# Kernel tuning notes

Hardware: AMD Instinct MI355X
Metric: run time of the kernel (lower is better)

Reference implementation:

```python
import jax, jax.numpy as jnp
import numpy as np

N_KNN = 16
BN_EPS = 1e-5


def conv1d(x, w, b):
    # x: (B,Cin,N), w: (Cout,Cin) -> (B,Cout,N)
    return jnp.einsum('oc,bcn->bon', w, x) + b[None, :, None]


def conv2d(x, w, b):
    # x: (B,Cin,N,K), w: (Cout,Cin) -> (B,Cout,N,K)
    return jnp.einsum('oc,bcnk->bonk', w, x) + b[None, :, None, None]


def bn2d(x, gamma, beta):
    # training-mode BatchNorm2d over (B,N,K) per channel
    mu = x.mean(axis=(0, 2, 3), keepdims=True)
    var = x.var(axis=(0, 2, 3), keepdims=True)
    return (x - mu) * jax.lax.rsqrt(var + BN_EPS) * gamma[None, :, None, None] + beta[None, :, None, None]


def knn_idx(pos, k):
    # pos: (B,3,N) -> (B,N,K) indices of k nearest neighbors (include_self=True)
    p = jnp.transpose(pos, (0, 2, 1))  # (B,N,3)
    sq = jnp.sum(p * p, axis=-1)  # (B,N)
    d = sq[:, :, None] + sq[:, None, :] - 2.0 * jnp.einsum('bnd,bmd->bnm', p, p)
    _, idx = jax.lax.top_k(-d, k)
    return idx


def group(feat, idx):
    # feat: (B,C,N), idx: (B,N,K) -> (B,C,N,K)
    return jnp.take_along_axis(feat[:, :, :, None], idx[:, None, :, :], axis=2)


def mlp_res(x, w1, b1, w2, b2, wsc, bsc):
    shortcut = conv1d(x, wsc, bsc)
    return conv1d(jax.nn.relu(conv1d(x, w1, b1)), w2, b2) + shortcut


def setup_inputs() -> dict:
    key0 = jax.random.key(0)
    ks = jax.random.split(key0, 16)
    B, N, C, D, PH = 2, 2048, 128, 256, 64
    AH = D * 4
    f = lambda i, shape: jax.random.normal(ks[i], shape, jnp.float32) * 0.02
    return dict(
        pos=jax.random.normal(ks[0], (B, 3, N), jnp.float32),
        key=jax.random.normal(ks[1], (B, C, N), jnp.float32),
        query=jax.random.normal(ks[2], (B, C, N), jnp.float32),
        mlp_w1=f(3, (C, 2 * C)), mlp_b1=jnp.zeros(C),
        mlp_w2=f(4, (C, C)), mlp_b2=jnp.zeros(C),
        mlp_wsc=f(5, (C, 2 * C)), mlp_bsc=jnp.zeros(C),
        wk=f(6, (D, C)), bk=jnp.zeros(D),
        wq=f(7, (D, C)), bq=jnp.zeros(D),
        wv=f(8, (D, C)), bv=jnp.zeros(D),
        pos_w1=f(9, (PH, 3)), pos_b1=jnp.zeros(PH),
        pos_g=jnp.ones(PH), pos_beta=jnp.zeros(PH),
        pos_w2=f(10, (D, PH)), pos_b2=jnp.zeros(D),
        attn_w1=f(11, (AH, D)), attn_b1=jnp.zeros(AH),
        attn_g=jnp.ones(AH), attn_beta=jnp.zeros(AH),
        attn_w2=f(12, (D, AH)), attn_b2=jnp.zeros(D),
        end_w=f(13, (C, D)), end_b=jnp.zeros(C),
    )


def reference(pos, key, query,
              mlp_w1, mlp_b1, mlp_w2, mlp_b2, mlp_wsc, mlp_bsc,
              wk, bk, wq, bq, wv, bv,
              pos_w1, pos_b1, pos_g, pos_beta, pos_w2, pos_b2,
              attn_w1, attn_b1, attn_g, attn_beta, attn_w2, attn_b2,
              end_w, end_b):
    # value = MLP_Res(cat(key, query))
    value = mlp_res(jnp.concatenate([key, query], axis=1),
                    mlp_w1, mlp_b1, mlp_w2, mlp_b2, mlp_wsc, mlp_bsc)
    identity = value
    k = conv1d(key, wk, bk)      # (B,D,N)
    q = conv1d(query, wq, bq)    # (B,D,N)
    v = conv1d(value, wv, bv)    # (B,D,N)

    idx = knn_idx(pos, N_KNN)    # (B,N,K)
    key_g = group(k, idx)        # (B,D,N,K)
    qk_rel = q[:, :, :, None] - key_g
    pos_rel = pos[:, :, :, None] - group(pos, idx)  # (B,3,N,K)

    # pos_mlp: conv2d -> BN -> ReLU -> conv2d
    h = jax.nn.relu(bn2d(conv2d(pos_rel, pos_w1, pos_b1), pos_g, pos_beta))
    pos_emb = conv2d(h, pos_w2, pos_b2)  # (B,D,N,K)

    # attn_mlp: conv2d -> BN -> ReLU -> conv2d, softmax over neighbor axis
    a = jax.nn.relu(bn2d(conv2d(qk_rel + pos_emb, attn_w1, attn_b1), attn_g, attn_beta))
    attn = jax.nn.softmax(conv2d(a, attn_w2, attn_b2), axis=-1)  # (B,D,N,K)

    val = v[:, :, :, None] + pos_emb
    agg = jnp.sum(attn * val, axis=-1)  # (B,D,N)
    y = conv1d(agg, end_w, end_b)
    return y + identity
```

## Files before the change

kernel.cpp:

```cpp
#include <hip/hip_runtime.h>
#include <hip/hip_bf16.h>
#include <math.h>

#define Bv 2
#define Nv 2048
#define Cv 128
#define Dv 256
#define PHv 64
#define AHv 1024
#define Kv 16
#define NSAMP (Bv*Nv*Kv)

typedef unsigned short ushortt;
typedef unsigned char u8;
typedef __attribute__((ext_vector_type(8))) short bf16x8;
typedef __attribute__((ext_vector_type(4))) float f32x4;

__device__ __forceinline__ float bf2f(ushortt h){
  union { unsigned int u; float f; } v; v.u = ((unsigned int)h) << 16; return v.f;
}
__device__ __forceinline__ ushortt f2bf(float f){
  union { unsigned int u; float f; } v; v.f = f;
  unsigned int r = v.u + 0x7FFFu + ((v.u >> 16) & 1u);
  return (ushortt)(r >> 16);
}
__device__ __forceinline__ u8 f2fp8(float f){
  union { float f; unsigned int u; } v; v.f = f;
  unsigned int s = (v.u >> 24) & 0x80u;
  unsigned int a = v.u & 0x7FFFFFFFu;
  if (a > 0x43E00000u) a = 0x43E00000u;
  unsigned int r = a + 0x7FFFFu + ((a >> 20) & 1u);
  int e = (int)((r >> 23) & 0xFF) - 120;
  unsigned int m = (r >> 20) & 7u;
  if (e <= 0) return (u8)s;
  return (u8)(s | ((unsigned)e << 3) | m);
}

__device__ __forceinline__ void gload16(const void* g, void* l){
  __builtin_amdgcn_global_load_lds(
      (const __attribute__((address_space(1))) unsigned int*)g,
      (__attribute__((address_space(3))) unsigned int*)l, 16, 0, 0);
}

__global__ __launch_bounds__(256) void prep_weights(
    const float* __restrict__ wk, const float* __restrict__ wq,
    const float* __restrict__ wv, const float* __restrict__ endw,
    const float* __restrict__ mw1, const float* __restrict__ mw2,
    const float* __restrict__ mwsc, const float* __restrict__ aw2,
    const float* __restrict__ pw2,
    ushortt* __restrict__ wA16, ushortt* __restrict__ wB16, ushortt* __restrict__ wv16,
    float* __restrict__ endwT, u8* __restrict__ w2f8, ushortt* __restrict__ pw2R)
{
  int tid = blockIdx.x*256 + threadIdx.x;
  int stride = gridDim.x*256;
  for (int i = tid; i < 768*256; i += stride){
    int r = i >> 8, c = i & 255;
    float v;
    if (r < 128) v = mw1[r*256 + c];
    else if (r < 384) v = (c < 128) ? wk[(r-128)*128 + c] : 0.f;
    else if (r < 640) v = (c >= 128) ? wq[(r-384)*128 + (c-128)] : 0.f;
    else v = 0.f;
    wA16[i] = f2bf(v);
  }
  for (int i = tid; i < 128*384; i += stride){
    int r = i / 384, c = i - r*384;
    float v = (c < 128) ? mw2[r*128 + c] : mwsc[r*256 + (c-128)];
    wB16[i] = f2bf(v);
  }
  for (int i = tid; i < 256*128; i += stride) wv16[i] = f2bf(wv[i]);
  for (int i = tid; i < 128*256; i += stride){ int co = i>>8, d = i&255; endwT[d*128+co] = endw[i]; }
  for (int i = tid; i < 256*1024; i += stride) w2f8[i] = f2fp8(aw2[i]*256.f);
  for (int i = tid; i < 256*64; i += stride) pw2R[i] = f2bf(pw2[i]);
}

__global__ __launch_bounds__(256) void xcat_kernel(
    const float* __restrict__ key, const float* __restrict__ query,
    ushortt* __restrict__ hx16)
{
  __shared__ float xs[256*33];
  int t = threadIdx.x;
  int tile = blockIdx.x & 63, b = blockIdx.x >> 6;
  int n0 = tile*32;
  for (int e = t; e < 256*32; e += 256){
    int c = e >> 5, nn = e & 31;
    xs[c*33+nn] = (c < 128) ? key[(size_t)(b*128+c)*Nv + n0+nn]
                            : query[(size_t)(b*128+(c-128))*Nv + n0+nn];
  }
  __syncthreads();
  int nn = t & 31, cg = t >> 5;
  size_t s = (size_t)b*Nv + n0 + nn;
  __align__(16) ushortt tmp[32];
  #pragma unroll
  for (int cc = 0; cc < 32; cc++) tmp[cc] = f2bf(xs[(cg*32+cc)*33 + nn]);
  uint4* dst = (uint4*)&hx16[s*384 + 128 + cg*32];
  #pragma unroll
  for (int q = 0; q < 4; q++) dst[q] = ((uint4*)tmp)[q];
}

__global__ __launch_bounds__(512) void gemmA_kernel(
    ushortt* __restrict__ hx16, const ushortt* __restrict__ wA16,
    const float* __restrict__ mb1, const float* __restrict__ bk, const float* __restrict__ bq,
    float* __restrict__ kT, float* __restrict__ qT)
{
  __shared__ ushortt As[128*64];
  __shared__ ushortt Bs[256*64];
  int t = threadIdx.x;
  int w = t >> 6, l = t & 63;
  int lr = l & 15, g4 = l >> 4;
  int wm = w >> 2, wn = w & 3;
  int s0 = blockIdx.x*128, n0 = blockIdx.y*256;

  f32x4 acc[4][4];
  #pragma unroll
  for (int i=0;i<4;i++) for (int j=0;j<4;j++) acc[i][j] = (f32x4){0.f,0.f,0.f,0.f};

  for (int kt = 0; kt < 4; kt++){
    int k0 = kt*64;
    __syncthreads();
    #pragma unroll
    for (int i = 0; i < 2; i++){
      int c = t + i*512;
      int r = c >> 3, db = (c & 7)*16;
      const ushortt* src = hx16 + (size_t)(s0+r)*384 + 128 + k0 + ((db ^ ((r&7)<<4))>>1);
      gload16(src, As + c*8);
    }
    #pragma unroll
    for (int i = 0; i < 4; i++){
      int c = t + i*512;
      int r = c >> 3, db = (c & 7)*16;
      const ushortt* src = wA16 + (size_t)(n0+r)*256 + k0 + ((db ^ ((r&7)<<4))>>1);
      gload16(src, Bs + c*8);
    }
    __syncthreads();
    #pragma unroll
    for (int kk = 0; kk < 2; kk++){
      int kb = kk*64 + g4*16;
      bf16x8 af[4];
      #pragma unroll
      for (int mi = 0; mi < 4; mi++){
        int row = wm*64 + mi*16 + lr;
        af[mi] = *(const bf16x8*)((const char*)As + row*128 + (kb ^ ((row&7)<<4)));
      }
      #pragma unroll
      for (int ni = 0; ni < 4; ni++){
        int row = wn*64 + ni*16 + lr;
        bf16x8 bfr = *(const bf16x8*)((const char*)Bs + row*128 + (kb ^ ((row&7)<<4)));
        #pragma unroll
        for (int mi = 0; mi < 4; mi++)
          acc[mi][ni] = __builtin_amdgcn_mfma_f32_16x16x32_bf16(af[mi], bfr, acc[mi][ni], 0,0,0);
      }
    }
  }
  #pragma unroll
  for (int ni = 0; ni < 4; ni++){
    int col = n0 + wn*64 + ni*16 + lr;
    if (col < 128){
      float bias = mb1[col];
      #pragma unroll
      for (int mi = 0; mi < 4; mi++){
        int rbase = s0 + wm*64 + mi*16 + g4*4;
        #pragma unroll
        for (int r = 0; r < 4; r++){
          float v = acc[mi][ni][r] + bias;
          v = v > 0.f ? v : 0.f;
          hx16[(size_t)(rbase+r)*384 + col] = f2bf(v);
        }
      }
    } else if (col < 384){
      float bias = bk[col-128];
      #pragma unroll
      for (int mi = 0; mi < 4; mi++){
        int rbase = s0 + wm*64 + mi*16 + g4*4;
        #pragma unroll
        for (int r = 0; r < 4; r++)
          kT[(size_t)(rbase+r)*256 + (col-128)] = acc[mi][ni][r] + bias;
      }
    } else if (col < 640){
      float bias = bq[col-384];
      #pragma unroll
      for (int mi = 0; mi < 4; mi++){
        int rbase = s0 + wm*64 + mi*16 + g4*4;
        #pragma unroll
        for (int r = 0; r < 4; r++)
          qT[(size_t)(rbase+r)*256 + (col-384)] = acc[mi][ni][r] + bias;
      }
    }
  }
}

__global__ __launch_bounds__(512) void gemmB_kernel(
    const ushortt* __restrict__ hx16, const ushortt* __restrict__ wB16,
    const float* __restrict__ mb2, const float* __restrict__ mbsc,
    float* __restrict__ valueT, ushortt* __restrict__ value16)
{
  __shared__ ushortt As[128*64];
  __shared__ ushortt Bs[128*64];
  int t = threadIdx.x;
  int w = t >> 6, l = t & 63;
  int lr = l & 15, g4 = l >> 4;
  int wm = w >> 2, wn = w & 3;
  int s0 = blockIdx.x*128;

  f32x4 acc[4][2];
  #pragma unroll
  for (int i=0;i<4;i++) for (int j=0;j<2;j++) acc[i][j] = (f32x4){0.f,0.f,0.f,0.f};

  for (int kt = 0; kt < 6; kt++){
    int k0 = kt*64;
    __syncthreads();
    #pragma unroll
    for (int i = 0; i < 2; i++){
      int c = t + i*512;
      int r = c >> 3, db = (c & 7)*16;
      const ushortt* src = hx16 + (size_t)(s0+r)*384 + k0 + ((db ^ ((r&7)<<4))>>1);
      gload16(src, As + c*8);
    }
    #pragma unroll
    for (int i = 0; i < 2; i++){
      int c = t + i*512;
      int r = c >> 3, db = (c & 7)*16;
      const ushortt* src = wB16 + (size_t)r*384 + k0 + ((db ^ ((r&7)<<4))>>1);
      gload16(src, Bs + c*8);
    }
    __syncthreads();
    #pragma unroll
    for (int kk = 0; kk < 2; kk++){
      int kb = kk*64 + g4*16;
      bf16x8 af[4];
      #pragma unroll
      for (int mi = 0; mi < 4; mi++){
        int row = wm*64 + mi*16 + lr;
        af[mi] = *(const bf16x8*)((const char*)As + row*128 + (kb ^ ((row&7)<<4)));
      }
      #pragma unroll
      for (int ni = 0; ni < 2; ni++){
        int row = wn*32 + ni*16 + lr;
        bf16x8 bfr = *(const bf16x8*)((const char*)Bs + row*128 + (kb ^ ((row&7)<<4)));
        #pragma unroll
        for (int mi = 0; mi < 4; mi++)
          acc[mi][ni] = __builtin_amdgcn_mfma_f32_16x16x32_bf16(af[mi], bfr, acc[mi][ni], 0,0,0);
      }
    }
  }
  #pragma unroll
  for (int ni = 0; ni < 2; ni++){
    int col = wn*32 + ni*16 + lr;
    float bias = mb2[col] + mbsc[col];
    #pragma unroll
    for (int mi = 0; mi < 4; mi++){
      int rbase = s0 + wm*64 + mi*16 + g4*4;
      #pragma unroll
      for (int r = 0; r < 4; r++){
        float v = acc[mi][ni][r] + bias;
        valueT[(size_t)(rbase+r)*128 + col] = v;
        value16[(size_t)(rbase+r)*128 + col] = f2bf(v);
      }
    }
  }
}

__global__ __launch_bounds__(512) void gemmC_kernel(
    const ushortt* __restrict__ value16, const ushortt* __restrict__ wv16,
    const float* __restrict__ bv, float* __restrict__ vT)
{
  __shared__ ushortt As[128*64];
  __shared__ ushortt Bs[256*64];
  int t = threadIdx.x;
  int w = t >> 6, l = t & 63;
  int lr = l & 15, g4 = l >> 4;
  int wm = w >> 2, wn = w & 3;
  int s0 = blockIdx.x*128;

  f32x4 acc[4][4];
  #pragma unroll
  for (int i=0;i<4;i++) for (int j=0;j<4;j++) acc[i][j] = (f32x4){0.f,0.f,0.f,0.f};

  for (int kt = 0; kt < 2; kt++){
    int k0 = kt*64;
    __syncthreads();
    #pragma unroll
    for (int i = 0; i < 2; i++){
      int c = t + i*512;
      int r = c >> 3, db = (c & 7)*16;
      const ushortt* src = value16 + (size_t)(s0+r)*128 + k0 + ((db ^ ((r&7)<<4))>>1);
      gload16(src, As + c*8);
    }
    #pragma unroll
    for (int i = 0; i < 4; i++){
      int c = t + i*512;
      int r = c >> 3, db = (c & 7)*16;
      const ushortt* src = wv16 + (size_t)r*128 + k0 + ((db ^ ((r&7)<<4))>>1);
      gload16(src, Bs + c*8);
    }
    __syncthreads();
    #pragma unroll
    for (int kk = 0; kk < 2; kk++){
      int kb = kk*64 + g4*16;
      bf16x8 af[4];
      #pragma unroll
      for (int mi = 0; mi < 4; mi++){
        int row = wm*64 + mi*16 + lr;
        af[mi] = *(const bf16x8*)((const char*)As + row*128 + (kb ^ ((row&7)<<4)));
      }
      #pragma unroll
      for (int ni = 0; ni < 4; ni++){
        int row = wn*64 + ni*16 + lr;
        bf16x8 bfr = *(const bf16x8*)((const char*)Bs + row*128 + (kb ^ ((row&7)<<4)));
        #pragma unroll
        for (int mi = 0; mi < 4; mi++)
          acc[mi][ni] = __builtin_amdgcn_mfma_f32_16x16x32_bf16(af[mi], bfr, acc[mi][ni], 0,0,0);
      }
    }
  }
  #pragma unroll
  for (int ni = 0; ni < 4; ni++){
    int col = wn*64 + ni*16 + lr;
    float bias = bv[col];
    #pragma unroll
    for (int mi = 0; mi < 4; mi++){
      int rbase = s0 + wm*64 + mi*16 + g4*4;
      #pragma unroll
      for (int r = 0; r < 4; r++)
        vT[(size_t)(rbase+r)*256 + col] = acc[mi][ni][r] + bias;
    }
  }
}

__global__ __launch_bounds__(256) void knn_kernel(const float* __restrict__ pos, int* __restrict__ idx)
{
  int t = threadIdx.x;
  int w = t >> 6, l = t & 63;
  int p = blockIdx.x*4 + w;
  int i = p & (Nv-1), b = p >> 11;
  const float* px = pos + (size_t)b*3*Nv;
  float pix = px[i], piy = px[Nv+i], piz = px[2*Nv+i];
  float sqi = pix*pix + piy*piy + piz*piz;
  float ds[32];
  #pragma unroll
  for (int jj = 0; jj < 32; jj++){
    int j = jj*64 + l;
    float qx = px[j], qy = px[Nv+j], qz = px[2*Nv+j];
    float sqj = qx*qx + qy*qy + qz*qz;
    float dot = pix*qx + piy*qy + piz*qz;
    ds[jj] = (sqi + sqj) - 2.0f*dot;
  }
  #pragma unroll 1
  for (int it = 0; it < 16; it++){
    float bv = 3.4e38f; int bj = 0x7FFFFFFF;
    #pragma unroll
    for (int jj = 0; jj < 32; jj++){
      int j = jj*64 + l;
      bool c = ds[jj] < bv;
      bv = c ? ds[jj] : bv;
      bj = c ? j : bj;
    }
    #pragma unroll
    for (int off = 32; off; off >>= 1){
      float ov = __shfl_xor(bv, off);
      int oj = __shfl_xor(bj, off);
      if (ov < bv || (ov == bv && oj < bj)){ bv = ov; bj = oj; }
    }
    if (l == 0) idx[(size_t)p*16 + it] = bj;
    #pragma unroll
    for (int jj = 0; jj < 32; jj++){
      if (jj*64 + l == bj) ds[jj] = 3.4e38f;
    }
  }
}

__global__ __launch_bounds__(256) void bn1_stats(const float* __restrict__ pos,
    const int* __restrict__ idx, float* __restrict__ rstat)
{
  int tid = blockIdx.x*256 + threadIdx.x;
  int stride = gridDim.x*256;
  float s[9] = {0,0,0,0,0,0,0,0,0};
  for (int e = tid; e < NSAMP; e += stride){
    int b = e >> 15;
    int rem = e & 32767;
    int n = rem >> 4, k = rem & 15;
    int j = idx[(size_t)(b*Nv+n)*16 + k];
    const float* px = pos + (size_t)b*3*Nv;
    float rx = px[n]-px[j], ry = px[Nv+n]-px[Nv+j], rz = px[2*Nv+n]-px[2*Nv+j];
    s[0]+=rx; s[1]+=ry; s[2]+=rz;
    s[3]+=rx*rx; s[4]+=rx*ry; s[5]+=rx*rz; s[6]+=ry*ry; s[7]+=ry*rz; s[8]+=rz*rz;
  }
  for (int off=32; off; off>>=1)
    for (int q=0;q<9;q++) s[q] += __shfl_xor(s[q], off);
  if ((threadIdx.x & 63) == 0)
    for (int q=0;q<9;q++) atomicAdd(&rstat[q], s[q]);
}

__global__ void bn1_final(const float* __restrict__ rstat,
    const float* __restrict__ pw1,
    const float* __restrict__ pg, const float* __restrict__ pbeta,
    float* __restrict__ w1eff, float* __restrict__ b1eff)
{
  int c = threadIdx.x;
  float inv = 1.0f/(float)NSAMP;
  float mux = rstat[0]*inv, muy = rstat[1]*inv, muz = rstat[2]*inv;
  float xx = rstat[3]*inv, xy = rstat[4]*inv, xz = rstat[5]*inv;
  float yy = rstat[6]*inv, yz = rstat[7]*inv, zz = rstat[8]*inv;
  float w0 = pw1[c*3], w1 = pw1[c*3+1], w2 = pw1[c*3+2];
  float dot = w0*mux + w1*muy + w2*muz;
  float quad = w0*w0*xx + w1*w1*yy + w2*w2*zz + 2.f*(w0*w1*xy + w0*w2*xz + w1*w2*yz);
  float var = quad - dot*dot;
  float s = pg[c] * rsqrtf(var + 1e-5f);
  w1eff[c*3]   = w0*s;
  w1eff[c*3+1] = w1*s;
  w1eff[c*3+2] = w2*s;
  b1eff[c] = pbeta[c] - dot*s;
}

__global__ __launch_bounds__(256) void hpos_kernel(
    const float* __restrict__ pos, const int* __restrict__ idx,
    const float* __restrict__ w1eff, const float* __restrict__ b1eff,
    ushortt* __restrict__ hposR)
{
  int t = threadIdx.x;
  int s = blockIdx.x*32 + (t>>3);
  int c0 = (t&7)*8;
  int ptv = s >> 4;
  int n = ptv & (Nv-1), b = ptv >> 11;
  int j = idx[s];
  const float* px = pos + (size_t)b*3*Nv;
  float rx = px[n]-px[j], ry = px[Nv+n]-px[Nv+j], rz = px[2*Nv+n]-px[2*Nv+j];
  ushortt outv[8];
  #pragma unroll
  for (int e = 0; e < 8; e++){
    int c = c0+e;
    float v = b1eff[c] + w1eff[c*3]*rx + w1eff[c*3+1]*ry + w1eff[c*3+2]*rz;
    outv[e] = f2bf(v > 0.f ? v : 0.f);
  }
  *(uint4*)&hposR[(size_t)s*64 + c0] = *(uint4*)outv;
}

__global__ __launch_bounds__(512) void gemm0_kernel(
    const ushortt* __restrict__ hposR, const ushortt* __restrict__ pw2R,
    const float* __restrict__ pb2, const int* __restrict__ idx,
    const float* __restrict__ qT, const float* __restrict__ kT, const float* __restrict__ vT,
    ushortt* __restrict__ U16, ushortt* __restrict__ val16, float* __restrict__ mu_sum)
{
  __shared__ ushortt As[128*64];
  __shared__ ushortt Bs[256*64];
  __shared__ float mured[8*256];
  int t = threadIdx.x;
  int w = t >> 6, l = t & 63;
  int lr = l & 15, g4 = l >> 4;
  int wm = w >> 2, wn = w & 3;
  int s0 = blockIdx.x*128;

  #pragma unroll
  for (int i = 0; i < 2; i++){
    int c = t + i*512;
    int r = c >> 3, db = (c & 7)*16;
    const ushortt* src = hposR + (size_t)(s0+r)*64 + ((db ^ ((r&7)<<4))>>1);
    gload16(src, As + c*8);
  }
  #pragma unroll
  for (int i = 0; i < 4; i++){
    int c = t + i*512;
    int r = c >> 3, db = (c & 7)*16;
    const ushortt* src = pw2R + (size_t)r*64 + ((db ^ ((r&7)<<4))>>1);
    gload16(src, Bs + c*8);
  }
  __syncthreads();

  f32x4 acc[4][4];
  #pragma unroll
  for (int i=0;i<4;i++) for (int j=0;j<4;j++) acc[i][j] = (f32x4){0.f,0.f,0.f,0.f};
  #pragma unroll
  for (int kk = 0; kk < 2; kk++){
    int kb = kk*64 + g4*16;
    bf16x8 af[4];
    #pragma unroll
    for (int mi = 0; mi < 4; mi++){
      int row = wm*64 + mi*16 + lr;
      af[mi] = *(const bf16x8*)((const char*)As + row*128 + (kb ^ ((row&7)<<4)));
    }
    #pragma unroll
    for (int ni = 0; ni < 4; ni++){
      int row = wn*64 + ni*16 + lr;
      bf16x8 bfr = *(const bf16x8*)((const char*)Bs + row*128 + (kb ^ ((row&7)<<4)));
      #pragma unroll
      for (int mi = 0; mi < 4; mi++)
        acc[mi][ni] = __builtin_amdgcn_mfma_f32_16x16x32_bf16(af[mi], bfr, acc[mi][ni], 0,0,0);
    }
  }

  float musum[4] = {0.f,0.f,0.f,0.f};
  __align__(16) float pb2v[4];
  #pragma unroll
  for (int ni = 0; ni < 4; ni++) pb2v[ni] = pb2[wn*64 + ni*16 + lr];
  #pragma unroll
  for (int mi = 0; mi < 4; mi++){
    #pragma unroll
    for (int r4 = 0; r4 < 4; r4++){
      int s = s0 + wm*64 + mi*16 + g4*4 + r4;
      int ptv = s >> 4;
      int b = s >> 15;
      int j = idx[s];
      const float* krow = kT + (size_t)(b*Nv + j)*256;
      const float* qrow = qT + (size_t)ptv*256;
      const float* vrow = vT + (size_t)ptv*256;
      #pragma unroll
      for (int ni = 0; ni < 4; ni++){
        int d = wn*64 + ni*16 + lr;
        float pe = acc[mi][ni][r4] + pb2v[ni];
        float u = qrow[d] - krow[d] + pe;
        U16[(size_t)s*256 + d] = f2bf(u);
        val16[(size_t)s*256 + d] = f2bf(vrow[d] + pe);
        musum[ni] += u;
      }
    }
  }
  #pragma unroll
  for (int ni = 0; ni < 4; ni++)
    mured[(wm*4+g4)*256 + wn*64 + ni*16 + lr] = musum[ni];
  __syncthreads();
  if (t < 256){
    float ssum = 0.f;
    #pragma unroll
    for (int q = 0; q < 8; q++) ssum += mured[q*256 + t];
    atomicAdd(&mu_sum[t], ssum);
  }
}

__global__ __launch_bounds__(512) void mm_kernel(const ushortt* __restrict__ U16,
                                                 ushortt* __restrict__ Mpart)
{
  __shared__ ushortt Ut[256*64];
  int t = threadIdx.x;
  int w = t >> 6, l = t & 63;
  int lr = l & 15, g4 = l >> 4;
  int wm = w >> 2, wn = w & 3;
  int c_my = ((w & 3)*64 + l);
  int sg = w >> 2;
  int blk = blockIdx.x;
  int sstart = blk*256;

  f32x4 acc[8][4];
  #pragma unroll
  for (int i=0;i<8;i++) for (int j=0;j<4;j++) acc[i][j] = (f32x4){0.f,0.f,0.f,0.f};

  for (int st = 0; st < 4; st++){
    int sb = sstart + st*64;
    __syncthreads();
    #pragma unroll
    for (int g = 0; g < 4; g++){
      int s8 = sg*32 + g*8;
      ushortt vals[8];
      #pragma unroll
      for (int e = 0; e < 8; e++)
        vals[e] = U16[(size_t)(sb + s8 + e)*256 + c_my];
      unsigned int p0 = (unsigned int)vals[0] | ((unsigned int)vals[1] << 16);
      unsigned int p1 = (unsigned int)vals[2] | ((unsigned int)vals[3] << 16);
      unsigned int p2 = (unsigned int)vals[4] | ((unsigned int)vals[5] << 16);
      unsigned int p3 = (unsigned int)vals[6] | ((unsigned int)vals[7] << 16);
      uint4 pk = make_uint4(p0,p1,p2,p3);
      *(uint4*)((char*)Ut + c_my*128 + ((s8*2) ^ ((c_my&7)<<4))) = pk;
    }
    __syncthreads();
    #pragma unroll
    for (int kk = 0; kk < 2; kk++){
      int kb = kk*64 + g4*16;
      bf16x8 af[8];
      #pragma unroll
      for (int ci = 0; ci < 8; ci++){
        int row = wm*128 + ci*16 + lr;
        af[ci] = *(const bf16x8*)((const char*)Ut + row*128 + (kb ^ ((row&7)<<4)));
      }
      #pragma unroll
      for (int cj = 0; cj < 4; cj++){
        int row = wn*64 + cj*16 + lr;
        bf16x8 bfr = *(const bf16x8*)((const char*)Ut + row*128 + (kb ^ ((row&7)<<4)));
        #pragma unroll
        for (int ci = 0; ci < 8; ci++)
          acc[ci][cj] = __builtin_amdgcn_mfma_f32_16x16x32_bf16(af[ci], bfr, acc[ci][cj], 0,0,0);
      }
    }
  }
  ushortt* dst = Mpart + (size_t)blk*65536;
  #pragma unroll
  for (int ci = 0; ci < 8; ci++){
    #pragma unroll
    for (int cj = 0; cj < 4; cj++){
      int c2 = wn*64 + cj*16 + lr;
      #pragma unroll
      for (int r = 0; r < 4; r++){
        int c1 = wm*128 + ci*16 + g4*4 + r;
        dst[(size_t)c1*256 + c2] = f2bf(acc[ci][cj][r]);
      }
    }
  }
}

__global__ __launch_bounds__(256) void mreduce_kernel(const ushortt* __restrict__ Mpart,
                                                      float* __restrict__ Mm)
{
  int i = blockIdx.x*256 + threadIdx.x;
  float s = 0.f;
  for (int p = 0; p < 256; p++) s += bf2f(Mpart[(size_t)p*65536 + i]);
  Mm[i] = s;
}

__global__ __launch_bounds__(256) void bn2_final(
    const float* __restrict__ Mm, const float* __restrict__ mu_sum,
    const float* __restrict__ aw1,
    const float* __restrict__ ag, const float* __restrict__ abeta,
    ushortt* __restrict__ w1R, float* __restrict__ b1eff2)
{
  __shared__ float wrow[256];
  __shared__ float red[8];
  __shared__ float s2s;
  int t = threadIdx.x;
  int ch = blockIdx.x;
  wrow[t] = aw1[(size_t)ch*256 + t];
  __syncthreads();
  float colacc = 0.f;
  for (int r = 0; r < 256; r++) colacc += wrow[r] * Mm[(size_t)r*256 + t];
  float inv = 1.0f/(float)NSAMP;
  float qpart = colacc * wrow[t] * inv;
  float dpart = wrow[t] * mu_sum[t] * inv;
  for (int off=32; off; off>>=1){ qpart += __shfl_xor(qpart, off); dpart += __shfl_xor(dpart, off); }
  if ((t&63)==0){ red[t>>6] = qpart; red[4 + (t>>6)] = dpart; }
  __syncthreads();
  if (t == 0){
    float quad = red[0]+red[1]+red[2]+red[3];
    float dot  = red[4]+red[5]+red[6]+red[7];
    float var = quad - dot*dot;
    float s2 = ag[ch] * rsqrtf(var + 1e-5f);
    b1eff2[ch] = abeta[ch] - dot*s2;
    s2s = s2;
  }
  __syncthreads();
  w1R[(size_t)ch*256 + t] = f2bf(wrow[t]*s2s);
}

__global__ __launch_bounds__(512) void gemm1_kernel(
    const ushortt* __restrict__ U16c, const ushortt* __restrict__ w1R,
    const float* __restrict__ b1eff2, u8* __restrict__ H)
{
  __shared__ ushortt As[128*64];
  __shared__ ushortt Bs[256*64];
  int t = threadIdx.x;
  int w = t >> 6, l = t & 63;
  int lr = l & 15, g4 = l >> 4;
  int wm = w >> 2, wn = w & 3;
  int s0 = blockIdx.x*128, n0 = blockIdx.y*256;

  f32x4 acc[4][4];
  #pragma unroll
  for (int i=0;i<4;i++) for (int j=0;j<4;j++) acc[i][j] = (f32x4){0.f,0.f,0.f,0.f};

  for (int kt = 0; kt < 4; kt++){
    int k0 = kt*64;
    __syncthreads();
    #pragma unroll
    for (int i = 0; i < 2; i++){
      int c = t + i*512;
      int r = c >> 3, db = (c & 7)*16;
      const ushortt* src = U16c + (size_t)(s0+r)*256 + k0 + ((db ^ ((r&7)<<4))>>1);
      gload16(src, As + c*8);
    }
    #pragma unroll
    for (int i = 0; i < 4; i++){
      int c = t + i*512;
      int r = c >> 3, db = (c & 7)*16;
      const ushortt* src = w1R + (size_t)(n0+r)*256 + k0 + ((db ^ ((r&7)<<4))>>1);
      gload16(src, Bs + c*8);
    }
    __syncthreads();
    #pragma unroll
    for (int kk = 0; kk < 2; kk++){
      int kb = kk*64 + g4*16;
      bf16x8 af[4];
      #pragma unroll
      for (int mi = 0; mi < 4; mi++){
        int row = wm*64 + mi*16 + lr;
        af[mi] = *(const bf16x8*)((const char*)As + row*128 + (kb ^ ((row&7)<<4)));
      }
      #pragma unroll
      for (int ni = 0; ni < 4; ni++){
        int row = wn*64 + ni*16 + lr;
        bf16x8 bfr = *(const bf16x8*)((const char*)Bs + row*128 + (kb ^ ((row&7)<<4)));
        #pragma unroll
        for (int mi = 0; mi < 4; mi++)
          acc[mi][ni] = __builtin_amdgcn_mfma_f32_16x16x32_bf16(af[mi], bfr, acc[mi][ni], 0,0,0);
      }
    }
  }
  __syncthreads();
  u8* rep = (u8*)Bs;
  #pragma unroll
  for (int ni = 0; ni < 4; ni++){
    int colc = wn*64 + ni*16 + lr;
    float bias = b1eff2[n0 + colc];
    #pragma unroll
    for (int mi = 0; mi < 4; mi++){
      int sloc = wm*64 + mi*16 + g4*4;
      #pragma unroll
      for (int r = 0; r < 4; r++){
        float v = acc[mi][ni][r] + bias;
        v = v > 0.f ? v : 0.f;
        rep[(sloc+r)*256 + colc] = f2fp8(4.f*v);
      }
    }
  }
  __syncthreads();
  #pragma unroll
  for (int i = 0; i < 4; i++){
    int e = t + i*512;
    int row = e >> 4, off = (e & 15)*16;
    *(uint4*)&H[(size_t)(s0+row)*1024 + n0 + off] = *(const uint4*)(rep + e*16);
  }
}

__global__ __launch_bounds__(512) void gemm2_kernel(
    const u8* __restrict__ H, const u8* __restrict__ w2f8,
    const float* __restrict__ ab2, const ushortt* __restrict__ val16,
    float* __restrict__ aggT, int s_off)
{
  __shared__ u8 As8[128*64];
  __shared__ u8 Bs8[256*64];
  int t = threadIdx.x;
  int w = t >> 6, l = t & 63;
  int lr = l & 15, g4 = l >> 4;
  int wm = w >> 2, wn = w & 3;
  int blk = blockIdx.x;
  int s0 = blk*128;

  f32x4 acc[4][4];
  #pragma unroll
  for (int i=0;i<4;i++) for (int j=0;j<4;j++) acc[i][j] = (f32x4){0.f,0.f,0.f,0.f};

  for (int kt = 0; kt < 16; kt++){
    int k0 = kt*64;
    __syncthreads();
    {
      int c = t;
      int r = c >> 2, db = (c & 3)*16;
      const u8* src = H + (size_t)(s0+r)*1024 + k0 + (db ^ ((r&3)<<4));
      gload16(src, As8 + c*16);
    }
    #pragma unroll
    for (int i = 0; i < 2; i++){
      int c = t + i*512;
      int r = c >> 2, db = (c & 3)*16;
      const u8* src = w2f8 + (size_t)r*1024 + k0 + (db ^ ((r&3)<<4));
      gload16(src, Bs8 + c*16);
    }
    __syncthreads();
    #pragma unroll
    for (int kk = 0; kk < 2; kk++){
      int kb = kk*32 + g4*8;
      long af[4];
      #pragma unroll
      for (int mi = 0; mi < 4; mi++){
        int row = wm*64 + mi*16 + lr;
        af[mi] = *(const long*)((const u8*)As8 + row*64 + (kb ^ ((row&3)<<4)));
      }
      #pragma unroll
      for (int ni = 0; ni < 4; ni++){
        int row = wn*64 + ni*16 + lr;
        long bfr = *(const long*)((const u8*)Bs8 + row*64 + (kb ^ ((row&3)<<4)));
        #pragma unroll
        for (int mi = 0; mi < 4; mi++)
          acc[mi][ni] = __builtin_amdgcn_mfma_f32_16x16x32_fp8_fp8(af[mi], bfr, acc[mi][ni], 0,0,0);
      }
    }
  }
  const float sc = 1.0f/1024.0f;
  int ptbase = s_off >> 4;
  #pragma unroll
  for (int mi = 0; mi < 4; mi++){
    int pt = ptbase + blk*8 + wm*4 + mi;
    int sbase = pt*16;
    #pragma unroll
    for (int ni = 0; ni < 4; ni++){
      int d = wn*64 + ni*16 + lr;
      float bias = ab2[d];
      float lg[4];
      #pragma unroll
      for (int r = 0; r < 4; r++) lg[r] = acc[mi][ni][r]*sc + bias;
      float mx = fmaxf(fmaxf(lg[0],lg[1]), fmaxf(lg[2],lg[3]));
      mx = fmaxf(mx, __shfl_xor(mx, 16));
      mx = fmaxf(mx, __shfl_xor(mx, 32));
      float ev[4], ss = 0.f;
      #pragma unroll
      for (int r = 0; r < 4; r++){ ev[r] = __expf(lg[r]-mx); ss += ev[r]; }
      ss += __shfl_xor(ss, 16);
      ss += __shfl_xor(ss, 32);
      float inv = 1.0f/ss;
      float pa = 0.f;
      #pragma unroll
      for (int r = 0; r < 4; r++){
        int s = sbase + g4*4 + r;
        pa += ev[r]*inv*bf2f(val16[(size_t)s*256 + d]);
      }
      pa += __shfl_xor(pa, 16);
      pa += __shfl_xor(pa, 32);
      if (g4 == 0) aggT[(size_t)pt*256 + d] = pa;
    }
  }
}

__global__ __launch_bounds__(256) void final_kernel(
    const float* __restrict__ aggT, const float* __restrict__ endwT,
    const float* __restrict__ endb, const float* __restrict__ valueT,
    float* __restrict__ out)
{
  __shared__ float ags[32*257];
  int t = threadIdx.x;
  int tile = blockIdx.x & 63, b = blockIdx.x >> 6;
  int n0 = tile*32;
  for (int e = t; e < 32*256; e += 256){
    int nn = e >> 8, d = e & 255;
    ags[nn*257 + d] = aggT[(size_t)(b*Nv + n0 + nn)*256 + d];
  }
  __syncthreads();
  int cg = t >> 2, ng = t & 3;
  int co0 = cg*2, nb = ng*8;
  float acc[2][8];
  for (int i=0;i<2;i++){ float bb = endb[co0+i]; for (int j=0;j<8;j++) acc[i][j]=bb; }
  for (int d = 0; d < 256; d++){
    float w0 = endwT[d*128 + co0], w1 = endwT[d*128 + co0 + 1];
    #pragma unroll
    for (int j=0;j<8;j++){
      float av = ags[(nb+j)*257 + d];
      acc[0][j] += w0*av; acc[1][j] += w1*av;
    }
  }
  for (int i=0;i<2;i++){
    for (int j=0;j<8;j++){
      int n = n0 + nb + j;
      size_t o = (size_t)(b*128 + co0 + i)*Nv + n;
      out[o] = acc[i][j] + valueT[(size_t)(b*Nv + n)*128 + co0 + i];
    }
  }
}

extern "C" void kernel_launch(void* const* d_in, const int* in_sizes, int n_in,
                              void* d_out, int out_size, void* d_ws, size_t ws_size,
                              hipStream_t stream)
{
  (void)in_sizes; (void)n_in; (void)out_size;
  const float* pos   = (const float*)d_in[0];
  const float* key   = (const float*)d_in[1];
  const float* query = (const float*)d_in[2];
  const float* mw1   = (const float*)d_in[3];
  const float* mb1   = (const float*)d_in[4];
  const float* mw2   = (const float*)d_in[5];
  const float* mb2   = (const float*)d_in[6];
  const float* mwsc  = (const float*)d_in[7];
  const float* mbsc  = (const float*)d_in[8];
  const float* wk    = (const float*)d_in[9];
  const float* bk    = (const float*)d_in[10];
  const float* wq    = (const float*)d_in[11];
  const float* bq    = (const float*)d_in[12];
  const float* wv    = (const float*)d_in[13];
  const float* bv    = (const float*)d_in[14];
  const float* pw1   = (const float*)d_in[15];
  const float* pg    = (const float*)d_in[17];
  const float* pbeta = (const float*)d_in[18];
  const float* pw2   = (const float*)d_in[19];
  const float* pb2   = (const float*)d_in[20];
  const float* aw1   = (const float*)d_in[21];
  const float* ag    = (const float*)d_in[23];
  const float* abeta = (const float*)d_in[24];
  const float* aw2   = (const float*)d_in[25];
  const float* ab2   = (const float*)d_in[26];
  const float* endw  = (const float*)d_in[27];
  const float* endb  = (const float*)d_in[28];
  float* out = (float*)d_out;

  char* wsb = (char*)d_ws;
  size_t off = 0;
  auto take = [&](size_t bytes)->char*{
    char* p = wsb + off; off += (bytes + 255) & ~(size_t)255; return p;
  };
  float* Mm      = (float*)take(65536*4);
  float* mu_sum  = (float*)take(256*4);
  float* rstat   = (float*)take(12*4);
  size_t zero_bytes = off;
  float* w1eff   = (float*)take(192*4);
  float* b1eff   = (float*)take(64*4);
  float* b1eff2  = (float*)take(1024*4);
  float* valueT  = (float*)take((size_t)524288*4);
  float* qT      = (float*)take((size_t)1048576*4);
  float* kT      = (float*)take((size_t)1048576*4);
  float* vT      = (float*)take((size_t)1048576*4);
  float* aggT    = (float*)take((size_t)1048576*4);
  float* endwT   = (float*)take(32768*4);
  int*   idxb    = (int*)take(65536*4);
  ushortt* hx16  = (ushortt*)take((size_t)4096*384*2);
  ushortt* value16=(ushortt*)take((size_t)524288*2);
  ushortt* wA16  = (ushortt*)take((size_t)768*256*2);
  ushortt* wB16  = (ushortt*)take((size_t)128*384*2);
  ushortt* wv16  = (ushortt*)take((size_t)256*128*2);
  ushortt* U16   = (ushortt*)take((size_t)16777216*2);
  ushortt* val16 = (ushortt*)take((size_t)16777216*2);
  ushortt* hposR = (ushortt*)take((size_t)4194304*2);
  ushortt* Mpart = (ushortt*)take((size_t)256*65536*2);
  ushortt* w1R   = (ushortt*)take((size_t)262144*2);
  u8*      w2f8  = (u8*)take((size_t)262144);
  ushortt* pw2R  = (ushortt*)take(16384*2);

  size_t avail = (ws_size > off) ? (ws_size - off) : 0;
  int nch = 1;
  while (nch < 64 && ((size_t)(NSAMP/nch))*1024 > avail) nch <<= 1;
  int chunk = NSAMP / nch;
  u8* H = (u8*)(wsb + off);

  hipMemsetAsync(d_ws, 0, zero_bytes, stream);
  prep_weights<<<512,256,0,stream>>>(wk,wq,wv,endw,mw1,mw2,mwsc,aw2,pw2,
                                     wA16,wB16,wv16,endwT,w2f8,pw2R);
  xcat_kernel<<<128,256,0,stream>>>(key,query,hx16);
  knn_kernel<<<1024,256,0,stream>>>(pos,idxb);
  gemmA_kernel<<<dim3(32,3),512,0,stream>>>(hx16,wA16,mb1,bk,bq,kT,qT);
  gemmB_kernel<<<32,512,0,stream>>>(hx16,wB16,mb2,mbsc,valueT,value16);
  gemmC_kernel<<<32,512,0,stream>>>(value16,wv16,bv,vT);
  bn1_stats<<<64,256,0,stream>>>(pos,idxb,rstat);
  bn1_final<<<1,64,0,stream>>>(rstat,pw1,pg,pbeta,w1eff,b1eff);
  hpos_kernel<<<2048,256,0,stream>>>(pos,idxb,w1eff,b1eff,hposR);
  gemm0_kernel<<<512,512,0,stream>>>(hposR,pw2R,pb2,idxb,qT,kT,vT,U16,val16,mu_sum);
  mm_kernel<<<256,512,0,stream>>>(U16,Mpart);
  mreduce_kernel<<<256,256,0,stream>>>(Mpart,Mm);
  bn2_final<<<1024,256,0,stream>>>(Mm,mu_sum,aw1,ag,abeta,w1R,b1eff2);
  for (int cc = 0; cc < nch; cc++){
    int s_off = cc*chunk;
    gemm1_kernel<<<dim3(chunk/128, 4),512,0,stream>>>(U16 + (size_t)s_off*256, w1R, b1eff2, H);
    gemm2_kernel<<<chunk/128,512,0,stream>>>(H, w2f8, ab2, val16, aggT, s_off);
  }
  final_kernel<<<128,256,0,stream>>>(aggT,endwT,endb,valueT,out);
}
```

Baseline: 310.8 us.

## Run attention first-layer GEMM in FP8 with scaled U and W1 operands

gemm0 now also writes an FP8 copy of the attention-MLP input U (scaled by 16), staged through shared memory for coalesced stores. bn2_final emits the BN-folded W1 as FP8 (scaled by 64), and gemm1 uses FP8 MFMA with the product rescaled by 1/1024. This halves operand bytes for the largest GEMM and uses the faster FP8 matrix path. It adds one extra 16M-byte write in gemm0 and a 1D grid remap intended to group blocks sharing tiles, at the cost of lower precision in the BN-normalised activations.

```diff
diff --git a/kernel.cpp b/kernel.cpp
--- a/kernel.cpp
+++ b/kernel.cpp
@@ -438,7 +438,8 @@
     const ushortt* __restrict__ hposR, const ushortt* __restrict__ pw2R,
     const float* __restrict__ pb2, const int* __restrict__ idx,
     const float* __restrict__ qT, const float* __restrict__ kT, const float* __restrict__ vT,
-    ushortt* __restrict__ U16, ushortt* __restrict__ val16, float* __restrict__ mu_sum)
+    ushortt* __restrict__ U16, u8* __restrict__ U8, ushortt* __restrict__ val16,
+    float* __restrict__ mu_sum)
 {
   __shared__ ushortt As[128*64];
   __shared__ ushortt Bs[256*64];
@@ -486,6 +487,8 @@
         acc[mi][ni] = __builtin_amdgcn_mfma_f32_16x16x32_bf16(af[mi], bfr, acc[mi][ni], 0,0,0);
     }
   }
+  __syncthreads();
+  u8* rep = (u8*)Bs;
 
   float musum[4] = {0.f,0.f,0.f,0.f};
   __align__(16) float pb2v[4];
@@ -495,7 +498,8 @@
   for (int mi = 0; mi < 4; mi++){
     #pragma unroll
     for (int r4 = 0; r4 < 4; r4++){
-      int s = s0 + wm*64 + mi*16 + g4*4 + r4;
+      int sloc = wm*64 + mi*16 + g4*4 + r4;
+      int s = s0 + sloc;
       int ptv = s >> 4;
       int b = s >> 15;
       int j = idx[s];
@@ -508,6 +512,7 @@
         float pe = acc[mi][ni][r4] + pb2v[ni];
         float u = qrow[d] - krow[d] + pe;
         U16[(size_t)s*256 + d] = f2bf(u);
+        rep[sloc*256 + d] = f2fp8(16.f*u);
         val16[(size_t)s*256 + d] = f2bf(vrow[d] + pe);
         musum[ni] += u;
       }
@@ -517,6 +522,12 @@
   for (int ni = 0; ni < 4; ni++)
     mured[(wm*4+g4)*256 + wn*64 + ni*16 + lr] = musum[ni];
   __syncthreads();
+  #pragma unroll
+  for (int i = 0; i < 4; i++){
+    int e = t + i*512;
+    int row = e >> 4, off = (e & 15)*16;
+    *(uint4*)&U8[(size_t)(s0+row)*256 + off] = *(const uint4*)(rep + e*16);
+  }
   if (t < 256){
     float ssum = 0.f;
     #pragma unroll
@@ -607,7 +618,7 @@
     const float* __restrict__ Mm, const float* __restrict__ mu_sum,
     const float* __restrict__ aw1,
     const float* __restrict__ ag, const float* __restrict__ abeta,
-    ushortt* __restrict__ w1R, float* __restrict__ b1eff2)
+    u8* __restrict__ w1f8, float* __restrict__ b1eff2)
 {
   __shared__ float wrow[256];
   __shared__ float red[8];
@@ -633,20 +644,25 @@
     s2s = s2;
   }
   __syncthreads();
-  w1R[(size_t)ch*256 + t] = f2bf(wrow[t]*s2s);
+  w1f8[(size_t)ch*256 + t] = f2fp8(64.f*wrow[t]*s2s);
 }
 
 __global__ __launch_bounds__(512) void gemm1_kernel(
-    const ushortt* __restrict__ U16c, const ushortt* __restrict__ w1R,
+    const u8* __restrict__ U8c, const u8* __restrict__ w1f8,
     const float* __restrict__ b1eff2, u8* __restrict__ H)
 {
-  __shared__ ushortt As[128*64];
-  __shared__ ushortt Bs[256*64];
+  __shared__ u8 arena[32768];
+  u8* As8 = arena;
+  u8* Bs8 = arena + 8192;
   int t = threadIdx.x;
   int w = t >> 6, l = t & 63;
   int lr = l & 15, g4 = l >> 4;
   int wm = w >> 2, wn = w & 3;
-  int s0 = blockIdx.x*128, n0 = blockIdx.y*256;
+  int nwg = gridDim.x;
+  int cpx = nwg >> 3;
+  int logical = (blockIdx.x & 7)*cpx + (blockIdx.x >> 3);
+  int mt = logical >> 2, nt = logical & 3;
+  int s0 = mt*128, n0 = nt*256;
 
   f32x4 acc[4][4];
   #pragma unroll
@@ -655,42 +671,42 @@
   for (int kt = 0; kt < 4; kt++){
     int k0 = kt*64;
     __syncthreads();
+    {
+      int c = t;
+      int r = c >> 2, db = (c & 3)*16;
+      const u8* src = U8c + (size_t)(s0+r)*256 + k0 + (db ^ ((r&3)<<4));
+      gload16(src, As8 + c*16);
+    }
     #pragma unroll
     for (int i = 0; i < 2; i++){
       int c = t + i*512;
-      int r = c >> 3, db = (c & 7)*16;
-      const ushortt* src = U16c + (size_t)(s0+r)*256 + k0 + ((db ^ ((r&7)<<4))>>1);
-      gload16(src, As + c*8);
-    }
-    #pragma unroll
-    for (int i = 0; i < 4; i++){
-      int c = t + i*512;
-      int r = c >> 3, db = (c & 7)*16;
-      const ushortt* src = w1R + (size_t)(n0+r)*256 + k0 + ((db ^ ((r&7)<<4))>>1);
-      gload16(src, Bs + c*8);
+      int r = c >> 2, db = (c & 3)*16;
+      const u8* src = w1f8 + (size_t)(n0+r)*256 + k0 + (db ^ ((r&3)<<4));
+      gload16(src, Bs8 + c*16);
     }
     __syncthreads();
     #pragma unroll
     for (int kk = 0; kk < 2; kk++){
-      int kb = kk*64 + g4*16;
-      bf16x8 af[4];
+      int kb = kk*32 + g4*8;
+      long af[4];
       #pragma unroll
       for (int mi = 0; mi < 4; mi++){
         int row = wm*64 + mi*16 + lr;
-        af[mi] = *(const bf16x8*)((const char*)As + row*128 + (kb ^ ((row&7)<<4)));
+        af[mi] = *(const long*)(As8 + row*64 + (kb ^ ((row&3)<<4)));
       }
       #pragma unroll
       for (int ni = 0; ni < 4; ni++){
         int row = wn*64 + ni*16 + lr;
-        bf16x8 bfr = *(const bf16x8*)((const char*)Bs + row*128 + (kb ^ ((row&7)<<4)));
+        long bfr = *(const long*)(Bs8 + row*64 + (kb ^ ((row&3)<<4)));
         #pragma unroll
         for (int mi = 0; mi < 4; mi++)
-          acc[mi][ni] = __builtin_amdgcn_mfma_f32_16x16x32_bf16(af[mi], bfr, acc[mi][ni], 0,0,0);
-      }
-    }
-  }
+          acc[mi][ni] = __builtin_amdgcn_mfma_f32_16x16x32_fp8_fp8(af[mi], bfr, acc[mi][ni], 0,0,0);
+      }
+    }
+  }
+  const float sc1 = 1.0f/1024.0f;
   __syncthreads();
-  u8* rep = (u8*)Bs;
+  u8* rep = arena;
   #pragma unroll
   for (int ni = 0; ni < 4; ni++){
     int colc = wn*64 + ni*16 + lr;
@@ -700,7 +716,7 @@
       int sloc = wm*64 + mi*16 + g4*4;
       #pragma unroll
       for (int r = 0; r < 4; r++){
-        float v = acc[mi][ni][r] + bias;
+        float v = acc[mi][ni][r]*sc1 + bias;
         v = v > 0.f ? v : 0.f;
         rep[(sloc+r)*256 + colc] = f2fp8(4.f*v);
       }
@@ -898,10 +914,11 @@
   ushortt* wB16  = (ushortt*)take((size_t)128*384*2);
   ushortt* wv16  = (ushortt*)take((size_t)256*128*2);
   ushortt* U16   = (ushortt*)take((size_t)16777216*2);
+  u8*      U8b   = (u8*)take((size_t)16777216);
   ushortt* val16 = (ushortt*)take((size_t)16777216*2);
   ushortt* hposR = (ushortt*)take((size_t)4194304*2);
   ushortt* Mpart = (ushortt*)take((size_t)256*65536*2);
-  ushortt* w1R   = (ushortt*)take((size_t)262144*2);
+  u8*      w1f8  = (u8*)take((size_t)262144);
   u8*      w2f8  = (u8*)take((size_t)262144);
   ushortt* pw2R  = (ushortt*)take(16384*2);
 
@@ -922,13 +939,13 @@
   bn1_stats<<<64,256,0,stream>>>(pos,idxb,rstat);
   bn1_final<<<1,64,0,stream>>>(rstat,pw1,pg,pbeta,w1eff,b1eff);
   hpos_kernel<<<2048,256,0,stream>>>(pos,idxb,w1eff,b1eff,hposR);
-  gemm0_kernel<<<512,512,0,stream>>>(hposR,pw2R,pb2,idxb,qT,kT,vT,U16,val16,mu_sum);
+  gemm0_kernel<<<512,512,0,stream>>>(hposR,pw2R,pb2,idxb,qT,kT,vT,U16,U8b,val16,mu_sum);
   mm_kernel<<<256,512,0,stream>>>(U16,Mpart);
   mreduce_kernel<<<256,256,0,stream>>>(Mpart,Mm);
-  bn2_final<<<1024,256,0,stream>>>(Mm,mu_sum,aw1,ag,abeta,w1R,b1eff2);
+  bn2_final<<<1024,256,0,stream>>>(Mm,mu_sum,aw1,ag,abeta,w1f8,b1eff2);
   for (int cc = 0; cc < nch; cc++){
     int s_off = cc*chunk;
-    gemm1_kernel<<<dim3(chunk/128, 4),512,0,stream>>>(U16 + (size_t)s_off*256, w1R, b1eff2, H);
+    gemm1_kernel<<<(chunk/128)*4,512,0,stream>>>(U8b + (size_t)s_off*256, w1f8, b1eff2, H);
     gemm2_kernel<<<chunk/128,512,0,stream>>>(H, w2f8, ab2, val16, aggT, s_off);
   }
   final_kernel<<<128,256,0,stream>>>(aggT,endwT,endb,valueT,out);
```

New measurement: 314.6 us. Within noise of the previous version (+1.2%).
